# Kernel tuning notes

Hardware: AMD Instinct MI355X
Metric: run time of the kernel (lower is better)

The kernel has to match this reference:

```python
import jax, jax.numpy as jnp
import numpy as np

B, C, H, W = 64, 512, 32, 32
D = C // 8  # 64


def setup_inputs() -> dict:
    key = jax.random.key(0)
    k1, k2, k3, k4 = jax.random.split(key, 4)
    x = jax.random.normal(k1, (B, C, H, W), dtype=jnp.float32)
    query_m = jax.random.normal(k2, (H * W, D), dtype=jnp.float32)
    key_m = jax.random.normal(k3, (H * W, D), dtype=jnp.float32)
    # 1x1 conv C->C: weight [C_out, C_in], kaiming-ish scale
    value_w = jax.random.normal(k4, (C, C), dtype=jnp.float32) * (1.0 / np.sqrt(C))
    value_b = jnp.zeros((C,), dtype=jnp.float32)
    return {"x": x, "query_m": query_m, "key_m": key_m,
            "value_w": value_w, "value_b": value_b}


def reference(x, query_m, key_m, value_w, value_b):
    b, c, h, w = x.shape
    xf = x.reshape(b, c, h * w)                        # [B, C, N]
    q = jnp.einsum('bcn,nd->bcd', xf, query_m)         # [B, C, D]
    k = jnp.einsum('bcn,nd->bcd', xf, key_m)           # [B, C, D]
    energy = jnp.einsum('bcd,bed->bce', q, k)          # [B, C, C]
    energy = jax.nn.sigmoid(energy)
    attention = jax.nn.softmax(energy, axis=-2)        # softmax over rows (dim=-2)
    # 1x1 conv = channel matmul + bias
    v = jnp.einsum('bcn,oc->bon', xf, value_w) + value_b[None, :, None]  # [B, C, N]
    # out[b,j,n] = sum_i v[b,i,n] * attention[b,i,j]
    out = jnp.einsum('bin,bij->bjn', v, attention)     # [B, C, N]
    return out.reshape(b, c, h, w)
```

## Files before the change

### kernel.cpp

```cpp
#include <hip/hip_runtime.h>

#define BK 32

typedef __attribute__((ext_vector_type(8))) short bf16x8;
typedef __attribute__((ext_vector_type(4))) float f32x4;

__device__ __forceinline__ unsigned short f2bf(float f) {
  unsigned u = __builtin_bit_cast(unsigned, f);
  unsigned r = (u + 0x7FFFu + ((u >> 16) & 1u)) >> 16;
  return (unsigned short)r;
}
__device__ __forceinline__ float bf2f(unsigned short h) {
  return __builtin_bit_cast(float, (unsigned)h << 16);
}
__device__ __forceinline__ unsigned pack2(unsigned short a, unsigned short b) {
  return (unsigned)a | ((unsigned)b << 16);
}

__device__ __forceinline__ void gld_lds16(const void* g, void* l) {
  __builtin_amdgcn_global_load_lds(
      (const __attribute__((address_space(1))) unsigned int*)g,
      (__attribute__((address_space(3))) unsigned int*)l, 16, 0, 0);
}

__device__ __forceinline__ void split8_store(float4 v0, float4 v1,
                                             unsigned short* Hdst,
                                             unsigned short* Ldst) {
  float f[8] = {v0.x, v0.y, v0.z, v0.w, v1.x, v1.y, v1.z, v1.w};
  unsigned short hh[8], ll[8];
#pragma unroll
  for (int i = 0; i < 8; ++i) {
    hh[i] = f2bf(f[i]);
    ll[i] = f2bf(f[i] - bf2f(hh[i]));
  }
  *reinterpret_cast<uint4*>(Hdst) = make_uint4(pack2(hh[0], hh[1]), pack2(hh[2], hh[3]),
                                               pack2(hh[4], hh[5]), pack2(hh[6], hh[7]));
  *reinterpret_cast<uint4*>(Ldst) = make_uint4(pack2(ll[0], ll[1]), pack2(ll[2], ll[3]),
                                               pack2(ll[4], ll[5]), pack2(ll[6], ll[7]));
}

__global__ __launch_bounds__(256) void qkm_split(const float* __restrict__ Qm,
                                                 const float* __restrict__ Km,
                                                 unsigned short* __restrict__ Th,
                                                 unsigned short* __restrict__ Tl) {
  __shared__ float lt[64][65];
  int k0 = blockIdx.x * 64;
  int half = blockIdx.y;
  const float* M = half ? Km : Qm;
  int t = threadIdx.x;
  int cl = (t & 15) * 4;
  int rl = t >> 4;
#pragma unroll
  for (int rr = 0; rr < 4; ++rr) {
    int r = rl + rr * 16;
    float4 v = *reinterpret_cast<const float4*>(&M[(long)(k0 + r) * 64 + cl]);
    lt[cl + 0][r] = v.x;
    lt[cl + 1][r] = v.y;
    lt[cl + 2][r] = v.z;
    lt[cl + 3][r] = v.w;
  }
  __syncthreads();
#pragma unroll
  for (int rr = 0; rr < 4; ++rr) {
    int c = rl + rr * 16;
    unsigned short h[4], lo[4];
#pragma unroll
    for (int i = 0; i < 4; ++i) {
      float f = lt[c][cl + i];
      h[i] = f2bf(f);
      lo[i] = f2bf(f - bf2f(h[i]));
    }
    *reinterpret_cast<uint2*>(&Th[(long)(half * 64 + c) * 1024 + k0 + cl]) =
        make_uint2(pack2(h[0], h[1]), pack2(h[2], h[3]));
    *reinterpret_cast<uint2*>(&Tl[(long)(half * 64 + c) * 1024 + k0 + cl]) =
        make_uint2(pack2(lo[0], lo[1]), pack2(lo[2], lo[3]));
  }
}

__global__ __launch_bounds__(256) void k1_mfma(const float* __restrict__ x,
                                               const unsigned short* __restrict__ Th,
                                               const unsigned short* __restrict__ Tl,
                                               float* __restrict__ qk) {
  __shared__ unsigned short Dh[2][128 * 32];
  __shared__ unsigned short Dl[2][128 * 32];
  __shared__ unsigned short Xh[2][64 * 32];
  __shared__ unsigned short Xl[2][64 * 32];
  const int t = threadIdx.x;
  const int l = t & 63;
  const int w = t >> 6;
  const int wr = w >> 1, wc = w & 1;
  const long mBase = (long)blockIdx.x * 64;

  f32x4 acc[4][2];
#pragma unroll
  for (int m = 0; m < 4; ++m)
#pragma unroll
    for (int n = 0; n < 2; ++n) acc[m][n] = (f32x4){0.f, 0.f, 0.f, 0.f};

  const int xrow_l = t >> 2;
  const int kslot = t & 3;
  const int xsl = kslot ^ ((t >> 3) & 3);
  const int srcslot = (l & 3) ^ ((l >> 3) & 3);
  const int frag_off = (l & 15) * 32 + ((((l >> 4) ^ (l >> 1)) & 3) * 8);
  const float* xrow = x + (mBase + xrow_l) * 1024;

#define K1_STAGE_B(k0, p)                                                     \
  {                                                                           \
    _Pragma("unroll") for (int c = 0; c < 2; ++c) {                           \
      int ch = c * 4 + w;                                                     \
      int row = ch * 16 + (l >> 2);                                           \
      gld_lds16(Th + (long)row * 1024 + (k0) + srcslot * 8, &Dh[p][ch * 512]);\
      gld_lds16(Tl + (long)row * 1024 + (k0) + srcslot * 8, &Dl[p][ch * 512]);\
    }                                                                         \
  }

#define K1_COMPUTE(p)                                                         \
  {                                                                           \
    bf16x8 dh[4], dl[4], xh[2], xl[2];                                        \
    _Pragma("unroll") for (int m = 0; m < 4; ++m) {                           \
      dh[m] = *reinterpret_cast<const bf16x8*>(&Dh[p][(wr * 64 + m * 16) * 32 + frag_off]); \
      dl[m] = *reinterpret_cast<const bf16x8*>(&Dl[p][(wr * 64 + m * 16) * 32 + frag_off]); \
    }                                                                         \
    _Pragma("unroll") for (int n = 0; n < 2; ++n) {                           \
      xh[n] = *reinterpret_cast<const bf16x8*>(&Xh[p][(wc * 32 + n * 16) * 32 + frag_off]); \
      xl[n] = *reinterpret_cast<const bf16x8*>(&Xl[p][(wc * 32 + n * 16) * 32 + frag_off]); \
    }                                                                         \
    _Pragma("unroll") for (int m = 0; m < 4; ++m)                             \
        _Pragma("unroll") for (int n = 0; n < 2; ++n) {                       \
      acc[m][n] = __builtin_amdgcn_mfma_f32_16x16x32_bf16(dh[m], xh[n], acc[m][n], 0, 0, 0); \
      acc[m][n] = __builtin_amdgcn_mfma_f32_16x16x32_bf16(dh[m], xl[n], acc[m][n], 0, 0, 0); \
      acc[m][n] = __builtin_amdgcn_mfma_f32_16x16x32_bf16(dl[m], xh[n], acc[m][n], 0, 0, 0); \
    }                                                                         \
  }

  {
    float4 p0 = *reinterpret_cast<const float4*>(&xrow[kslot * 8]);
    float4 p1 = *reinterpret_cast<const float4*>(&xrow[kslot * 8 + 4]);
    K1_STAGE_B(0, 0);
    split8_store(p0, p1, &Xh[0][xrow_l * 32 + xsl * 8], &Xl[0][xrow_l * 32 + xsl * 8]);
  }

  for (int k0 = 0; k0 < 1024; k0 += 64) {
    __syncthreads();
    float4 na0 = *reinterpret_cast<const float4*>(&xrow[k0 + 32 + kslot * 8]);
    float4 na1 = *reinterpret_cast<const float4*>(&xrow[k0 + 32 + kslot * 8 + 4]);
    K1_STAGE_B(k0 + 32, 1);
    K1_COMPUTE(0);
    split8_store(na0, na1, &Xh[1][xrow_l * 32 + xsl * 8], &Xl[1][xrow_l * 32 + xsl * 8]);
    __syncthreads();
    if (k0 + 64 < 1024) {
      float4 nb0 = *reinterpret_cast<const float4*>(&xrow[k0 + 64 + kslot * 8]);
      float4 nb1 = *reinterpret_cast<const float4*>(&xrow[k0 + 64 + kslot * 8 + 4]);
      K1_STAGE_B(k0 + 64, 0);
      K1_COMPUTE(1);
      split8_store(nb0, nb1, &Xh[0][xrow_l * 32 + xsl * 8], &Xl[0][xrow_l * 32 + xsl * 8]);
    } else {
      K1_COMPUTE(1);
    }
  }

#pragma unroll
  for (int m = 0; m < 4; ++m)
#pragma unroll
    for (int n = 0; n < 2; ++n) {
      int d0 = wr * 64 + m * 16 + (l >> 4) * 4;
      long xr = mBase + wc * 32 + n * 16 + (l & 15);
      *reinterpret_cast<float4*>(&qk[xr * 128 + d0]) =
          make_float4(acc[m][n][0], acc[m][n][1], acc[m][n][2], acc[m][n][3]);
    }
#undef K1_STAGE_B
#undef K1_COMPUTE
}

__global__ __launch_bounds__(256) void k2a_mfma(const float* __restrict__ qk,
                                                unsigned short* __restrict__ st) {
  __shared__ unsigned short Ah[128 * 32];
  __shared__ unsigned short Al[128 * 32];
  __shared__ unsigned short Bh[128 * 32];
  __shared__ unsigned short Bl[128 * 32];
  const int t = threadIdx.x;
  const int l = t & 63;
  const int w = t >> 6;
  const int wr = w >> 1, wc = w & 1;

  const int cpx = gridDim.x >> 3;
  const int orig = blockIdx.x;
  const int lw = (orig & 7) * cpx + (orig >> 3);
  const int b = lw >> 4;
  const int tile = lw & 15;
  const int iBase = (tile >> 2) * 128;
  const int jBase = (tile & 3) * 128;
  const float* qb = qk + (long)b * 512 * 128;

  f32x4 acc[4][4];
#pragma unroll
  for (int m = 0; m < 4; ++m)
#pragma unroll
    for (int n = 0; n < 4; ++n) acc[m][n] = (f32x4){0.f, 0.f, 0.f, 0.f};

  const int r0 = t >> 2;
  const int kslot = t & 3;
  const int sl = kslot ^ ((t >> 3) & 3);
  const int frag_off = (l & 15) * 32 + ((((l >> 4) ^ (l >> 1)) & 3) * 8);

  for (int d0 = 0; d0 < 64; d0 += BK) {
    __syncthreads();
#pragma unroll
    for (int h = 0; h < 2; ++h) {
      int row = r0 + h * 64;
      const float* qa = &qb[(long)(iBase + row) * 128 + d0 + kslot * 8];
      float4 a0 = *reinterpret_cast<const float4*>(qa);
      float4 a1 = *reinterpret_cast<const float4*>(qa + 4);
      split8_store(a0, a1, &Ah[row * 32 + sl * 8], &Al[row * 32 + sl * 8]);
      const float* kb = &qb[(long)(jBase + row) * 128 + 64 + d0 + kslot * 8];
      float4 b0 = *reinterpret_cast<const float4*>(kb);
      float4 b1 = *reinterpret_cast<const float4*>(kb + 4);
      split8_store(b0, b1, &Bh[row * 32 + sl * 8], &Bl[row * 32 + sl * 8]);
    }
    __syncthreads();

    bf16x8 ah[4], al4[4], bh[4], bl4[4];
#pragma unroll
    for (int m = 0; m < 4; ++m) {
      ah[m] = *reinterpret_cast<const bf16x8*>(&Ah[(wr * 64 + m * 16) * 32 + frag_off]);
      al4[m] = *reinterpret_cast<const bf16x8*>(&Al[(wr * 64 + m * 16) * 32 + frag_off]);
    }
#pragma unroll
    for (int n = 0; n < 4; ++n) {
      bh[n] = *reinterpret_cast<const bf16x8*>(&Bh[(wc * 64 + n * 16) * 32 + frag_off]);
      bl4[n] = *reinterpret_cast<const bf16x8*>(&Bl[(wc * 64 + n * 16) * 32 + frag_off]);
    }
#pragma unroll
    for (int m = 0; m < 4; ++m)
#pragma unroll
      for (int n = 0; n < 4; ++n) {
        acc[m][n] = __builtin_amdgcn_mfma_f32_16x16x32_bf16(ah[m], bh[n], acc[m][n], 0, 0, 0);
        acc[m][n] = __builtin_amdgcn_mfma_f32_16x16x32_bf16(ah[m], bl4[n], acc[m][n], 0, 0, 0);
        acc[m][n] = __builtin_amdgcn_mfma_f32_16x16x32_bf16(al4[m], bh[n], acc[m][n], 0, 0, 0);
      }
  }
  unsigned short* sb = st + (long)b * 512 * 512;
#pragma unroll
  for (int m = 0; m < 4; ++m)
#pragma unroll
    for (int n = 0; n < 4; ++n) {
      int i0 = iBase + wr * 64 + m * 16 + (l >> 4) * 4;
      int j = jBase + wc * 64 + n * 16 + (l & 15);
      unsigned short p[4];
#pragma unroll
      for (int reg = 0; reg < 4; ++reg) {
        float sg = 1.0f / (1.0f + __expf(-acc[m][n][reg]));
        p[reg] = f2bf(__expf(sg));
      }
      *reinterpret_cast<uint2*>(&sb[(long)j * 512 + i0]) = *reinterpret_cast<uint2*>(p);
    }
}

__global__ __launch_bounds__(256) void k2b_rsum(const unsigned short* __restrict__ st,
                                                const float* __restrict__ bias,
                                                float* __restrict__ rsum,
                                                float* __restrict__ attbias) {
  int jg = blockIdx.x * 4 + (threadIdx.x >> 6);
  int l = threadIdx.x & 63;
  const unsigned short* row = st + (long)jg * 512 + l * 8;
  ushort4 u0 = *reinterpret_cast<const ushort4*>(row);
  ushort4 u1 = *reinterpret_cast<const ushort4*>(row + 4);
  float4 b0 = *reinterpret_cast<const float4*>(&bias[l * 8]);
  float4 b1 = *reinterpret_cast<const float4*>(&bias[l * 8 + 4]);
  float f0 = bf2f(u0.x), f1 = bf2f(u0.y), f2 = bf2f(u0.z), f3 = bf2f(u0.w);
  float f4 = bf2f(u1.x), f5 = bf2f(u1.y), f6 = bf2f(u1.z), f7 = bf2f(u1.w);
  float sum = (f0 + f1) + (f2 + f3) + ((f4 + f5) + (f6 + f7));
  float sumb = f0 * b0.x + f1 * b0.y + f2 * b0.z + f3 * b0.w +
               f4 * b1.x + f5 * b1.y + f6 * b1.z + f7 * b1.w;
#pragma unroll
  for (int off = 32; off > 0; off >>= 1) {
    sum += __shfl_down(sum, off);
    sumb += __shfl_down(sumb, off);
  }
  if (l == 0) {
    float r = 1.0f / sum;
    rsum[jg] = r;
    attbias[jg] = sumb * r;
  }
}

__global__ __launch_bounds__(256) void transpose_conv(const float* __restrict__ in,
                                                      unsigned short* __restrict__ out,
                                                      int inRows, int inCols,
                                                      long inBatch, long outBatch) {
  __shared__ unsigned short lt[64][65];
  int b = blockIdx.z;
  int r0 = blockIdx.y * 64;
  int c0 = blockIdx.x * 64;
  const float* I = in + (long)b * inBatch;
  unsigned short* O = out + (long)b * outBatch;
  int t = threadIdx.x;
  int cl = (t & 15) * 4;
  int rl = t >> 4;
#pragma unroll
  for (int rr = 0; rr < 4; ++rr) {
    int r = rl + rr * 16;
    float4 v = *reinterpret_cast<const float4*>(&I[(long)(r0 + r) * inCols + c0 + cl]);
    lt[cl + 0][r] = f2bf(v.x);
    lt[cl + 1][r] = f2bf(v.y);
    lt[cl + 2][r] = f2bf(v.z);
    lt[cl + 3][r] = f2bf(v.w);
  }
  __syncthreads();
#pragma unroll
  for (int rr = 0; rr < 4; ++rr) {
    int c = rl + rr * 16;
    unsigned short v[4] = {lt[c][cl], lt[c][cl + 1], lt[c][cl + 2], lt[c][cl + 3]};
    *reinterpret_cast<uint2*>(&O[(long)(c0 + c) * inRows + r0 + cl]) =
        *reinterpret_cast<uint2*>(&v[0]);
  }
}

template <int MODE>
__global__ __launch_bounds__(512) void mfma_nt256(const unsigned short* __restrict__ Abase,
                                                  const unsigned short* __restrict__ Bbase,
                                                  const float* __restrict__ rowscale,
                                                  unsigned short* __restrict__ Wout,
                                                  float* __restrict__ Fout) {
  __shared__ unsigned short As[2][256 * 64];
  __shared__ unsigned short Bs[2][256 * 64];
  const int t = threadIdx.x;
  const int l = t & 63;
  const int w = t >> 6;
  const int wr = w >> 2;
  const int wc = w & 3;

  const int cpx = gridDim.x >> 3;
  const int orig = blockIdx.x;
  const int lw = (orig & 7) * cpx + (orig >> 3);
  const int TPB_SH = (MODE == 0) ? 2 : 3;
  const int b = lw >> TPB_SH;
  const int tile = lw & ((1 << TPB_SH) - 1);
  const int mBase = (tile >> 1) * 256;
  const int nBase = (tile & 1) * 256;

  const unsigned short* Ag = Abase + ((MODE == 0) ? 0L : (long)b * (1024 * 512)) + (long)mBase * 512;
  const unsigned short* Bg = Bbase + (long)b * (512 * 512) + (long)nBase * 512;

  f32x4 acc[8][4];
#pragma unroll
  for (int m = 0; m < 8; ++m)
#pragma unroll
    for (int n = 0; n < 4; ++n) acc[m][n] = (f32x4){0.f, 0.f, 0.f, 0.f};

  const int srcslot = (l & 7) ^ (l >> 3);

#define NT_STAGE(kt, p)                                                        \
  {                                                                            \
    _Pragma("unroll") for (int pr = 0; pr < 4; ++pr) {                         \
      int rr = pr * 64 + w * 8 + (l >> 3);                                     \
      gld_lds16(Ag + (long)rr * 512 + (kt) * 64 + srcslot * 8,                 \
                &As[p][(pr * 64 + w * 8) * 64]);                               \
      gld_lds16(Bg + (long)rr * 512 + (kt) * 64 + srcslot * 8,                 \
                &Bs[p][(pr * 64 + w * 8) * 64]);                               \
    }                                                                          \
  }

#define NT_COMPUTE(p)                                                          \
  {                                                                            \
    _Pragma("unroll") for (int kk = 0; kk < 2; ++kk) {                         \
      const int so = ((kk * 4 + (l >> 4)) ^ (l & 7)) * 8;                      \
      bf16x8 af[8], bfr[4];                                                    \
      _Pragma("unroll") for (int m = 0; m < 8; ++m)                            \
        af[m] = *reinterpret_cast<const bf16x8*>(                              \
            &As[p][(wr * 128 + m * 16 + (l & 15)) * 64 + so]);                 \
      _Pragma("unroll") for (int n = 0; n < 4; ++n)                            \
        bfr[n] = *reinterpret_cast<const bf16x8*>(                             \
            &Bs[p][(wc * 64 + n * 16 + (l & 15)) * 64 + so]);                  \
      _Pragma("unroll") for (int m = 0; m < 8; ++m)                            \
        _Pragma("unroll") for (int n = 0; n < 4; ++n)                          \
          acc[m][n] = __builtin_amdgcn_mfma_f32_16x16x32_bf16(af[m], bfr[n],   \
                                                              acc[m][n], 0, 0, 0); \
    }                                                                          \
  }

  NT_STAGE(0, 0);
  __syncthreads();
  for (int kt = 0; kt < 6; kt += 2) {
    NT_STAGE(kt + 1, 1);
    NT_COMPUTE(0);
    __syncthreads();
    NT_STAGE(kt + 2, 0);
    NT_COMPUTE(1);
    __syncthreads();
  }
  NT_STAGE(7, 1);
  NT_COMPUTE(0);
  __syncthreads();
  NT_COMPUTE(1);
#undef NT_STAGE
#undef NT_COMPUTE

  if (MODE == 0) {
    unsigned short* W = Wout + (long)b * (512 * 512);
#pragma unroll
    for (int n = 0; n < 4; ++n) {
      int j = nBase + wc * 64 + n * 16 + (l & 15);
      float rs = rowscale[b * 512 + j];
#pragma unroll
      for (int m = 0; m < 8; ++m) {
        int c0 = mBase + wr * 128 + m * 16 + (l >> 4) * 4;
        unsigned short p[4];
#pragma unroll
        for (int reg = 0; reg < 4; ++reg) p[reg] = f2bf(acc[m][n][reg] * rs);
        *reinterpret_cast<uint2*>(&W[(long)j * 512 + c0]) = *reinterpret_cast<uint2*>(p);
      }
    }
  } else {
    float* O = Fout + (long)b * (512 * 1024);
#pragma unroll
    for (int n = 0; n < 4; ++n) {
      int j = nBase + wc * 64 + n * 16 + (l & 15);
      float ab = rowscale[b * 512 + j];
#pragma unroll
      for (int m = 0; m < 8; ++m) {
        int n0 = mBase + wr * 128 + m * 16 + (l >> 4) * 4;
        *reinterpret_cast<float4*>(&O[(long)j * 1024 + n0]) =
            make_float4(acc[m][n][0] + ab, acc[m][n][1] + ab,
                        acc[m][n][2] + ab, acc[m][n][3] + ab);
      }
    }
  }
}

extern "C" void kernel_launch(void* const* d_in, const int* in_sizes, int n_in,
                              void* d_out, int out_size, void* d_ws, size_t ws_size,
                              hipStream_t stream) {
  const float* x  = (const float*)d_in[0];
  const float* Qm = (const float*)d_in[1];
  const float* Km = (const float*)d_in[2];
  const float* vw = (const float*)d_in[3];
  const float* vb = (const float*)d_in[4];
  float* out = (float*)d_out;

  float* ws = (float*)d_ws;
  float* qk = ws;
  unsigned short* st   = (unsigned short*)(ws + 4194304);
  unsigned short* weff = (unsigned short*)(ws + 4194304 + 8388608);
  unsigned short* xbT  = (unsigned short*)(ws + 4194304 + 16777216);
  unsigned short* vwT  = (unsigned short*)(ws + 4194304 + 33554432);
  unsigned short* qkTh = (unsigned short*)(ws + 4194304 + 33554432 + 131072);
  unsigned short* qkTl = qkTh + 131072;
  float* rsum    = ws + 4194304 + 33554432 + 131072 + 131072;
  float* attbias = rsum + 32768;

  transpose_conv<<<dim3(16, 8, 64), 256, 0, stream>>>(x, xbT, 512, 1024, 524288L, 524288L);
  transpose_conv<<<dim3(8, 8, 1), 256, 0, stream>>>(vw, vwT, 512, 512, 0L, 0L);
  qkm_split<<<dim3(16, 2), 256, 0, stream>>>(Qm, Km, qkTh, qkTl);
  k1_mfma<<<512, 256, 0, stream>>>(x, qkTh, qkTl, qk);
  k2a_mfma<<<1024, 256, 0, stream>>>(qk, st);
  k2b_rsum<<<8192, 256, 0, stream>>>(st, vb, rsum, attbias);
  mfma_nt256<0><<<256, 512, 0, stream>>>(vwT, st, rsum, weff, nullptr);
  mfma_nt256<1><<<512, 512, 0, stream>>>(xbT, weff, attbias, nullptr, out);
}
```

Measured before the change: 225.6 us.

## Load full K-depth in k2a and deepen NT GEMM prefetch with explicit waitcnt

The k2a energy kernel now stages the whole 64-deep Q/K tile into shared memory once, using an XOR swizzle, instead of looping over two K-chunks with extra barriers. The NT GEMM main loop is restructured to keep two stages in flight. It uses explicit vmcnt waits, raw s_barrier wrapped in sched_barrier, and setprio around the MFMA compute so global-to-LDS loads overlap compute more deeply. This trades higher LDS use in k2a and hand-tuned wait counts, which are fragile if the per-stage load count is not 8, for fewer synchronizations and better latency hiding.

```diff
diff --git a/kernel.cpp b/kernel.cpp
--- a/kernel.cpp
+++ b/kernel.cpp
@@ -22,6 +22,10 @@
       (const __attribute__((address_space(1))) unsigned int*)g,
       (__attribute__((address_space(3))) unsigned int*)l, 16, 0, 0);
 }
+
+#define SCHED0() __builtin_amdgcn_sched_barrier(0)
+#define NTBAR() do { SCHED0(); __builtin_amdgcn_s_barrier(); SCHED0(); } while (0)
+#define VMW(N) do { asm volatile("s_waitcnt vmcnt(" #N ")" ::: "memory"); SCHED0(); } while (0)
 
 __device__ __forceinline__ void split8_store(float4 v0, float4 v1,
                                              unsigned short* Hdst,
@@ -174,10 +178,10 @@
 
 __global__ __launch_bounds__(256) void k2a_mfma(const float* __restrict__ qk,
                                                 unsigned short* __restrict__ st) {
-  __shared__ unsigned short Ah[128 * 32];
-  __shared__ unsigned short Al[128 * 32];
-  __shared__ unsigned short Bh[128 * 32];
-  __shared__ unsigned short Bl[128 * 32];
+  __shared__ unsigned short Ah[128 * 64];
+  __shared__ unsigned short Al[128 * 64];
+  __shared__ unsigned short Bh[128 * 64];
+  __shared__ unsigned short Bl[128 * 64];
   const int t = threadIdx.x;
   const int l = t & 63;
   const int w = t >> 6;
@@ -192,43 +196,46 @@
   const int jBase = (tile & 3) * 128;
   const float* qb = qk + (long)b * 512 * 128;
 
+  {
+    const int r = t >> 1;
+    const int kh = t & 1;
+    const float* qa = &qb[(long)(iBase + r) * 128 + kh * 32];
+    const float* kb = &qb[(long)(jBase + r) * 128 + 64 + kh * 32];
+#pragma unroll
+    for (int c = 0; c < 4; ++c) {
+      int s = (kh * 4 + c) ^ (r & 7);
+      float4 a0 = *reinterpret_cast<const float4*>(&qa[c * 8]);
+      float4 a1 = *reinterpret_cast<const float4*>(&qa[c * 8 + 4]);
+      split8_store(a0, a1, &Ah[r * 64 + s * 8], &Al[r * 64 + s * 8]);
+      float4 b0 = *reinterpret_cast<const float4*>(&kb[c * 8]);
+      float4 b1 = *reinterpret_cast<const float4*>(&kb[c * 8 + 4]);
+      split8_store(b0, b1, &Bh[r * 64 + s * 8], &Bl[r * 64 + s * 8]);
+    }
+  }
+  __syncthreads();
+
   f32x4 acc[4][4];
 #pragma unroll
   for (int m = 0; m < 4; ++m)
 #pragma unroll
     for (int n = 0; n < 4; ++n) acc[m][n] = (f32x4){0.f, 0.f, 0.f, 0.f};
 
-  const int r0 = t >> 2;
-  const int kslot = t & 3;
-  const int sl = kslot ^ ((t >> 3) & 3);
-  const int frag_off = (l & 15) * 32 + ((((l >> 4) ^ (l >> 1)) & 3) * 8);
-
-  for (int d0 = 0; d0 < 64; d0 += BK) {
-    __syncthreads();
-#pragma unroll
-    for (int h = 0; h < 2; ++h) {
-      int row = r0 + h * 64;
-      const float* qa = &qb[(long)(iBase + row) * 128 + d0 + kslot * 8];
-      float4 a0 = *reinterpret_cast<const float4*>(qa);
-      float4 a1 = *reinterpret_cast<const float4*>(qa + 4);
-      split8_store(a0, a1, &Ah[row * 32 + sl * 8], &Al[row * 32 + sl * 8]);
-      const float* kb = &qb[(long)(jBase + row) * 128 + 64 + d0 + kslot * 8];
-      float4 b0 = *reinterpret_cast<const float4*>(kb);
-      float4 b1 = *reinterpret_cast<const float4*>(kb + 4);
-      split8_store(b0, b1, &Bh[row * 32 + sl * 8], &Bl[row * 32 + sl * 8]);
-    }
-    __syncthreads();
-
+#pragma unroll
+  for (int ks = 0; ks < 2; ++ks) {
     bf16x8 ah[4], al4[4], bh[4], bl4[4];
 #pragma unroll
     for (int m = 0; m < 4; ++m) {
-      ah[m] = *reinterpret_cast<const bf16x8*>(&Ah[(wr * 64 + m * 16) * 32 + frag_off]);
-      al4[m] = *reinterpret_cast<const bf16x8*>(&Al[(wr * 64 + m * 16) * 32 + frag_off]);
+      int row = wr * 64 + m * 16 + (l & 15);
+      int off = row * 64 + ((ks * 4 + (l >> 4)) ^ (row & 7)) * 8;
+      ah[m] = *reinterpret_cast<const bf16x8*>(&Ah[off]);
+      al4[m] = *reinterpret_cast<const bf16x8*>(&Al[off]);
     }
 #pragma unroll
     for (int n = 0; n < 4; ++n) {
-      bh[n] = *reinterpret_cast<const bf16x8*>(&Bh[(wc * 64 + n * 16) * 32 + frag_off]);
-      bl4[n] = *reinterpret_cast<const bf16x8*>(&Bl[(wc * 64 + n * 16) * 32 + frag_off]);
+      int row = wc * 64 + n * 16 + (l & 15);
+      int off = row * 64 + ((ks * 4 + (l >> 4)) ^ (row & 7)) * 8;
+      bh[n] = *reinterpret_cast<const bf16x8*>(&Bh[off]);
+      bl4[n] = *reinterpret_cast<const bf16x8*>(&Bl[off]);
     }
 #pragma unroll
     for (int m = 0; m < 4; ++m)
@@ -239,6 +246,7 @@
         acc[m][n] = __builtin_amdgcn_mfma_f32_16x16x32_bf16(al4[m], bh[n], acc[m][n], 0, 0, 0);
       }
   }
+
   unsigned short* sb = st + (long)b * 512 * 512;
 #pragma unroll
   for (int m = 0; m < 4; ++m)
@@ -380,19 +388,24 @@
   }
 
   NT_STAGE(0, 0);
-  __syncthreads();
-  for (int kt = 0; kt < 6; kt += 2) {
-    NT_STAGE(kt + 1, 1);
-    NT_COMPUTE(0);
-    __syncthreads();
-    NT_STAGE(kt + 2, 0);
-    NT_COMPUTE(1);
-    __syncthreads();
-  }
-  NT_STAGE(7, 1);
-  NT_COMPUTE(0);
-  __syncthreads();
-  NT_COMPUTE(1);
+  NT_STAGE(1, 1);
+  VMW(8);
+  NTBAR();
+
+  for (int kt = 0; kt < 8; ++kt) {
+    const int p = kt & 1;
+    __builtin_amdgcn_s_setprio(1);
+    NT_COMPUTE(p);
+    __builtin_amdgcn_s_setprio(0);
+    NTBAR();
+    if (kt < 6) {
+      NT_STAGE(kt + 2, p);
+      VMW(8);
+    } else {
+      VMW(0);
+    }
+    NTBAR();
+  }
 #undef NT_STAGE
 #undef NT_COMPUTE
 
```

Result: no change. 221.4 us (-1.8%).
